# Kernel tuning notes

Measured on AMD Instinct MI355X. Metric: run time of the kernel, lower is better.

The kernel has to match this reference:

```python
import jax, jax.numpy as jnp
import numpy as np

B, S, D = 8, 2048, 768
H1 = 512
EMBED_DIM = 768  # scale = sqrt(embed_dim)


def setup_inputs() -> dict:
    key = jax.random.key(0)
    ks = jax.random.split(key, 5)
    q = jax.random.normal(ks[0], (B, S, D), dtype=jnp.float32)
    k = jax.random.normal(ks[1], (B, S, D), dtype=jnp.float32)
    v = jax.random.normal(ks[2], (B, S, D), dtype=jnp.float32)
    W1 = jax.random.normal(ks[3], (D, H1), dtype=jnp.float32) * (1.0 / np.sqrt(D))
    b1 = jnp.zeros((H1,), dtype=jnp.float32)
    W2 = jax.random.normal(ks[4], (H1, 1), dtype=jnp.float32) * (1.0 / np.sqrt(H1))
    b2 = jnp.zeros((1,), dtype=jnp.float32)
    return {"q": q, "k": k, "v": v, "W1": W1, "b1": b1, "W2": W2, "b2": b2}


def reference(q, k, v, W1, b1, W2, b2):
    # MLP gate on v: fc2(tanh(fc1(v))) -> [B, S, 1] -> squeeze -> [B, S]
    g = jnp.tanh(v @ W1 + b1) @ W2 + b2          # [B, S, 1]
    g = g[..., 0][:, None, :]                    # unsqueeze(-2): [B, 1, S]

    # scores scaled by sqrt(seq_len) (q.shape[1]), as in the original
    scores = jnp.einsum("bqd,bkd->bqk", q, k) / jnp.sqrt(
        jnp.asarray(q.shape[1], dtype=q.dtype))  # [B, S, S]

    # first softmax over dim=1 (column-wise over query axis)
    s = jax.nn.softmax(scores, axis=1)           # [B, S, S]

    # blend with column-mean, scale by sqrt(embed_dim)
    s_mean = jnp.mean(s, axis=1, keepdims=True)  # [B, 1, S]
    scale = jnp.sqrt(jnp.asarray(EMBED_DIM, dtype=q.dtype))
    attn_scores = (s * (1.0 - g) + s_mean * g) / scale

    # second softmax over last dim; dropout p=0 is identity
    attn_weights = jax.nn.softmax(attn_scores, axis=-1)

    attn_output = jnp.einsum("bqk,bkd->bqd", attn_weights, v) + q
    return attn_output, attn_weights
```

## Files before the change

### kernel.cpp

```cpp
#include <hip/hip_runtime.h>

#define BATCH 8
#define SEQ   2048
#define DIM   768
#define HID   512

typedef __attribute__((ext_vector_type(8))) short  short8;
typedef __attribute__((ext_vector_type(4))) float  f32x4;

#define BAR()   asm volatile("s_barrier" ::: "memory")
#define WAITL0() asm volatile("s_waitcnt lgkmcnt(0)" ::: "memory")
#define VMC(n)  asm volatile("s_waitcnt vmcnt(" #n ")" ::: "memory")

__device__ __forceinline__ unsigned short f2bf(float f) {
  union { float f; unsigned u; } x; x.f = f;
  return (unsigned short)((x.u + 0x7FFFu + ((x.u >> 16) & 1u)) >> 16);
}
__device__ __forceinline__ float bf2f(unsigned short u) {
  union { unsigned u; float f; } x; x.u = ((unsigned)u) << 16;
  return x.f;
}
__device__ __forceinline__ void gll16(const void* g, void* l) {
  __builtin_amdgcn_global_load_lds(
      (const __attribute__((address_space(1))) void*)g,
      (__attribute__((address_space(3))) void*)l, 16, 0, 0);
}
__device__ __forceinline__ int swz2(int o) { return o ^ (((o >> 8) & 7) << 4); }
__device__ __forceinline__ int swz3(int o) { return o ^ (((o >> 7) & 7) << 4); }

template<int VAR>
__global__ __launch_bounds__(512, 2)
void gemm8(const unsigned short* __restrict__ Ap, const unsigned short* __restrict__ Bp,
           const float* __restrict__ qres, float* __restrict__ Cf)
{
  constexpr int K     = (VAR == 1) ? DIM : SEQ;
  constexpr int NT    = K / 64;
  constexpr int NITER = NT / 2;
  constexpr int APB   = (VAR == 1) ? DIM * 2 : SEQ * 2;
  constexpr int BPB   = (VAR == 1) ? 8192    : SEQ * 2;
  constexpr int GX    = (VAR == 1) ? 8 : 3;
  constexpr int GY    = 8;
  constexpr int NWG   = GX * GY * BATCH;

  __shared__ __align__(16) unsigned char LDS[131072];

  int wg = ((blockIdx.x & 7) * (NWG >> 3)) + ((int)blockIdx.x >> 3);
  const int z  = wg / (GX * GY);
  const int r2 = wg % (GX * GY);
  const int by = r2 / GX;
  const int bx = r2 % GX;
  const int brow = by * 256, bcol = bx * 256;

  const int tid  = threadIdx.x;
  const int lane = tid & 63, wid = tid >> 6;
  const int wm   = wid >> 2, wn = wid & 3;
  const int lhi  = lane >> 4, llo = lane & 15;

  const char* Abase;
  const char* Bbase;
  if constexpr (VAR == 1) {
    Abase = (const char*)(Ap + (size_t)z * SEQ * DIM) + (size_t)brow * APB;
    Bbase = (const char*)(Bp + (size_t)z * SEQ * 4096 + 2048) + (size_t)bcol * BPB;
  } else {
    Abase = (const char*)(Ap + (size_t)z * SEQ * SEQ) + (size_t)brow * APB;
    Bbase = (const char*)(Bp + (size_t)z * (size_t)DIM * SEQ) + (size_t)bcol * BPB;
  }

  int sr[2], sk[2];
  #pragma unroll
  for (int c = 0; c < 2; ++c) {
    int o = wid * 2048 + c * 1024 + lane * 16;
    int a = swz3(o);
    sr[c] = a >> 7; sk[c] = a & 127;
  }
  auto stA = [&](int buf, int hh, int t) {
    #pragma unroll
    for (int c = 0; c < 2; ++c)
      gll16(Abase + (size_t)(hh * 128 + sr[c]) * APB + t * 128 + sk[c],
            LDS + buf * 32768 + hh * 16384 + wid * 2048 + c * 1024);
  };
  auto stB = [&](int buf, int hh, int t) {
    #pragma unroll
    for (int c = 0; c < 2; ++c)
      gll16(Bbase + (size_t)(hh * 128 + sr[c]) * BPB + t * 128 + sk[c],
            LDS + 65536 + buf * 32768 + hh * 16384 + wid * 2048 + c * 1024);
  };

  f32x4 acc[8][4];
  #pragma unroll
  for (int m = 0; m < 8; ++m)
    #pragma unroll
    for (int n = 0; n < 4; ++n)
      acc[m][n] = (f32x4)(0.0f);

  stA(0, 0, 0); stA(0, 1, 0); stB(0, 0, 0); stB(0, 1, 0);
  stB(1, 0, 1); stB(1, 1, 1);
  VMC(4);
  BAR();

  auto ITER = [&](int i, bool last) {
    #pragma unroll
    for (int kk = 0; kk < 2; ++kk) {
      const int buf = kk;
      short8 aR[4][2], b0R[2][2], b1R[2][2];
      #pragma unroll
      for (int ph = 0; ph < 4; ++ph) {
        const int h  = ph >> 1;
        const int nh = (ph == 1 || ph == 2) ? 1 : 0;
        if (ph == 0 || ph == 2) {
          #pragma unroll
          for (int fm = 0; fm < 4; ++fm)
            #pragma unroll
            for (int kh = 0; kh < 2; ++kh) {
              int o = (wm * 128 + h * 64 + fm * 16 + llo) * 128 + kh * 64 + lhi * 16;
              aR[fm][kh] = *(const short8*)(LDS + buf * 32768 + swz3(o));
            }
        }
        if (ph == 0) {
          #pragma unroll
          for (int fn = 0; fn < 2; ++fn)
            #pragma unroll
            for (int kh = 0; kh < 2; ++kh) {
              int o = (wn * 64 + fn * 16 + llo) * 128 + kh * 64 + lhi * 16;
              b0R[fn][kh] = *(const short8*)(LDS + 65536 + buf * 32768 + swz3(o));
            }
        }
        if (ph == 1) {
          #pragma unroll
          for (int fn = 0; fn < 2; ++fn)
            #pragma unroll
            for (int kh = 0; kh < 2; ++kh) {
              int o = (wn * 64 + 32 + fn * 16 + llo) * 128 + kh * 64 + lhi * 16;
              b1R[fn][kh] = *(const short8*)(LDS + 65536 + buf * 32768 + swz3(o));
            }
        }
        const int P = kk * 4 + ph;
        if      (P == 0) stA(1, 0, 2 * i + 1);
        else if (P == 1) stA(1, 1, 2 * i + 1);
        else if (P == 2) { if (!last) stB(0, 0, 2 * i + 2); }
        else if (P == 3) { if (!last) stB(0, 1, 2 * i + 2); }
        else if (P == 4) { if (!last) stA(0, 0, 2 * i + 2); }
        else if (P == 5) { if (!last) stA(0, 1, 2 * i + 2); }
        else if (P == 6) { if (!last) stB(1, 0, 2 * i + 3); }
        else if (P == 7) { if (!last) stB(1, 1, 2 * i + 3); }
        if (P == 3) { if (last) { VMC(0); } else { VMC(4); } }
        if (P == 7) { if (!last) { VMC(4); } }
        BAR();
        WAITL0();
        __builtin_amdgcn_sched_barrier(0);
        __builtin_amdgcn_s_setprio(1);
        #pragma unroll
        for (int kh = 0; kh < 2; ++kh)
          #pragma unroll
          for (int fm = 0; fm < 4; ++fm)
            #pragma unroll
            for (int fn = 0; fn < 2; ++fn)
              acc[h * 4 + fm][nh * 2 + fn] = __builtin_amdgcn_mfma_f32_16x16x32_bf16(
                  aR[fm][kh], nh ? b1R[fn][kh] : b0R[fn][kh],
                  acc[h * 4 + fm][nh * 2 + fn], 0, 0, 0);
        __builtin_amdgcn_s_setprio(0);
        BAR();
      }
    }
  };

  for (int i = 0; i < NITER - 1; ++i) ITER(i, false);
  ITER(NITER - 1, true);

  if constexpr (VAR == 1) {
    const float rs = 0.02209708691207961f;
    unsigned short* C16 = reinterpret_cast<unsigned short*>(Cf);
    #pragma unroll
    for (int FM = 0; FM < 8; ++FM)
      #pragma unroll
      for (int r = 0; r < 4; ++r) {
        size_t R = (size_t)z * SEQ + (brow + wm * 128 + FM * 16 + lhi * 4 + r);
        #pragma unroll
        for (int FN = 0; FN < 4; ++FN) {
          int col = bcol + wn * 64 + FN * 16 + llo;
          C16[R * 4096 + col] = f2bf(acc[FM][FN][r] * rs);
        }
      }
  }
  if constexpr (VAR == 2) {
    float* C = Cf + (size_t)z * SEQ * DIM;
    const float* Q = qres + (size_t)z * SEQ * DIM;
    #pragma unroll
    for (int FM = 0; FM < 8; ++FM)
      #pragma unroll
      for (int r = 0; r < 4; ++r) {
        int rowg = brow + wm * 128 + FM * 16 + lhi * 4 + r;
        #pragma unroll
        for (int FN = 0; FN < 4; ++FN) {
          int colg = bcol + wn * 64 + FN * 16 + llo;
          C[(size_t)rowg * DIM + colg] = acc[FM][FN][r] + Q[(size_t)rowg * DIM + colg];
        }
      }
  }
}

__global__ __launch_bounds__(256)
void gemm_gate(const unsigned short* __restrict__ Ab, const unsigned short* __restrict__ Bb,
               const float* __restrict__ bias, const float* __restrict__ W2,
               float* __restrict__ pg)
{
  constexpr int K = DIM, NT = K / 32, APITCH = 4096, BPITCH = DIM;
  constexpr int GX = 4, NWG = 512;

  __shared__ __align__(16) unsigned short AsL[2 * 128 * 32];
  __shared__ __align__(16) unsigned short BsL[2 * 128 * 32];
  __shared__ float gred[128][2];

  int wg = blockIdx.x;
  wg = (wg & 7) * (NWG >> 3) + (wg >> 3);
  const int bx = wg % GX;
  const int by = wg / GX;

  const int tid  = threadIdx.x;
  const int brow = by * 128;
  const int bcol = bx * 128;
  const int lane = tid & 63;
  const int wid  = tid >> 6;
  const int wr   = (wid >> 1) * 64;
  const int wc   = (wid & 1) * 64;
  const int lhi  = lane >> 4;
  const int llo  = lane & 15;

  const unsigned short* Asrc = Ab + (size_t)brow * APITCH;
  const unsigned short* Bsrc = Bb + (size_t)bcol * BPITCH;

  f32x4 acc[4][4];
  #pragma unroll
  for (int m = 0; m < 4; ++m)
    #pragma unroll
    for (int n = 0; n < 4; ++n)
      acc[m][n] = (f32x4)(0.0f);

  auto stage = [&](int buf, int k0) {
    #pragma unroll
    for (int i = 0; i < 2; ++i) {
      int ob = wid * 2048 + i * 1024;
      int a  = swz2(ob + lane * 16);
      gll16((const char*)Asrc + (size_t)(a >> 6) * (APITCH * 2) + (size_t)k0 * 2 + (a & 63),
            (char*)AsL + buf * 8192 + ob);
    }
    #pragma unroll
    for (int i = 0; i < 2; ++i) {
      int ob = wid * 2048 + i * 1024;
      int a  = swz2(ob + lane * 16);
      gll16((const char*)Bsrc + (size_t)(a >> 6) * (BPITCH * 2) + (size_t)k0 * 2 + (a & 63),
            (char*)BsL + buf * 8192 + ob);
    }
  };

  stage(0, 0);
  for (int t = 0; t < NT; ++t) {
    if (t + 1 < NT) {
      stage((t + 1) & 1, (t + 1) * 32);
      VMC(4);
    } else {
      VMC(0);
    }
    BAR();
    __builtin_amdgcn_sched_barrier(0);

    const int bb = (t & 1) * 8192;
    short8 af[4], bfr[4];
    #pragma unroll
    for (int m = 0; m < 4; ++m) {
      int a = (wr + m * 16 + llo) * 64 + lhi * 16;
      af[m] = *(const short8*)((const char*)AsL + bb + swz2(a));
    }
    #pragma unroll
    for (int n = 0; n < 4; ++n) {
      int a = (wc + n * 16 + llo) * 64 + lhi * 16;
      bfr[n] = *(const short8*)((const char*)BsL + bb + swz2(a));
    }
    #pragma unroll
    for (int m = 0; m < 4; ++m)
      #pragma unroll
      for (int n = 0; n < 4; ++n)
        acc[m][n] = __builtin_amdgcn_mfma_f32_16x16x32_bf16(af[m], bfr[n], acc[m][n], 0, 0, 0);

    __builtin_amdgcn_sched_barrier(0);
    BAR();
    __builtin_amdgcn_sched_barrier(0);
  }

  #pragma unroll
  for (int m = 0; m < 4; ++m) {
    #pragma unroll
    for (int r = 0; r < 4; ++r) {
      int lrow = wr + m * 16 + lhi * 4 + r;
      float part = 0.f;
      #pragma unroll
      for (int n = 0; n < 4; ++n) {
        int colg = bcol + wc + n * 16 + llo;
        float t = tanhf(acc[m][n][r] + bias[colg]);
        part += t * W2[colg];
      }
      part += __shfl_xor(part, 1);
      part += __shfl_xor(part, 2);
      part += __shfl_xor(part, 4);
      part += __shfl_xor(part, 8);
      if (llo == 0) gred[lrow][wid & 1] = part;
    }
  }
  __syncthreads();
  if (tid < 128)
    pg[(size_t)bx * 16384 + brow + tid] = gred[tid][0] + gred[tid][1];
}

__global__ __launch_bounds__(256)
void gemm_slow(const float* __restrict__ Wf, const float* __restrict__ Vf,
               const float* __restrict__ qres, float* __restrict__ Cf)
{
  __shared__ __align__(16) unsigned short AsL[128 * 64];
  __shared__ __align__(16) unsigned short BsL[128 * 32];

  const int tid  = threadIdx.x;
  const int z    = blockIdx.z;
  const int brow = blockIdx.y * 128;
  const int bcol = blockIdx.x * 128;
  const int lane = tid & 63;
  const int wid  = tid >> 6;
  const int wr   = (wid >> 1) * 64;
  const int wc   = (wid & 1) * 64;
  const int lhi  = lane >> 4;
  const int llo  = lane & 15;

  const float* AsrcF = Wf + (size_t)z * SEQ * SEQ + (size_t)brow * SEQ;
  const float* BsrcF = Vf + (size_t)z * SEQ * DIM;

  f32x4 acc[4][4];
  #pragma unroll
  for (int m = 0; m < 4; ++m)
    #pragma unroll
    for (int n = 0; n < 4; ++n)
      acc[m][n] = (f32x4)(0.0f);

  for (int k0 = 0; k0 < SEQ; k0 += 32) {
    #pragma unroll
    for (int i = 0; i < 4; ++i) {
      int ob = wid * 4096 + i * 1024;
      int a  = swz3(ob + lane * 16);
      gll16((const char*)AsrcF + (size_t)(a >> 7) * (SEQ * 4) + (size_t)k0 * 4 + (a & 127),
            (char*)AsL + ob);
    }
    {
      int n4 = (tid & 31) << 2;
      int kb = (tid >> 5) << 2;
      float4 r0 = *(const float4*)(BsrcF + (size_t)(k0 + kb + 0) * DIM + bcol + n4);
      float4 r1 = *(const float4*)(BsrcF + (size_t)(k0 + kb + 1) * DIM + bcol + n4);
      float4 r2 = *(const float4*)(BsrcF + (size_t)(k0 + kb + 2) * DIM + bcol + n4);
      float4 r3 = *(const float4*)(BsrcF + (size_t)(k0 + kb + 3) * DIM + bcol + n4);
      float a0[4] = {r0.x, r0.y, r0.z, r0.w};
      float a1[4] = {r1.x, r1.y, r1.z, r1.w};
      float a2[4] = {r2.x, r2.y, r2.z, r2.w};
      float a3[4] = {r3.x, r3.y, r3.z, r3.w};
      #pragma unroll
      for (int jj = 0; jj < 4; ++jj) {
        unsigned lo = (__float_as_uint(a0[jj]) >> 16) | (__float_as_uint(a1[jj]) & 0xFFFF0000u);
        unsigned hi = (__float_as_uint(a2[jj]) >> 16) | (__float_as_uint(a3[jj]) & 0xFFFF0000u);
        int ol = (n4 + jj) * 64 + kb * 2;
        *(uint2*)((char*)BsL + swz2(ol)) = make_uint2(lo, hi);
      }
    }
    __syncthreads();

    short8 af[4], bfr[4];
    #pragma unroll
    for (int m = 0; m < 4; ++m) {
      int row = wr + m * 16 + llo;
      int a0i = row * 128 + lhi * 32;
      f32x4 x = *(const f32x4*)((const char*)AsL + swz3(a0i));
      f32x4 y = *(const f32x4*)((const char*)AsL + swz3(a0i + 16));
      union { unsigned u[4]; short8 s; } r;
      r.u[0] = (__float_as_uint(x[0]) >> 16) | (__float_as_uint(x[1]) & 0xFFFF0000u);
      r.u[1] = (__float_as_uint(x[2]) >> 16) | (__float_as_uint(x[3]) & 0xFFFF0000u);
      r.u[2] = (__float_as_uint(y[0]) >> 16) | (__float_as_uint(y[1]) & 0xFFFF0000u);
      r.u[3] = (__float_as_uint(y[2]) >> 16) | (__float_as_uint(y[3]) & 0xFFFF0000u);
      af[m] = r.s;
    }
    #pragma unroll
    for (int n = 0; n < 4; ++n) {
      int a = (wc + n * 16 + llo) * 64 + lhi * 16;
      bfr[n] = *(const short8*)((const char*)BsL + swz2(a));
    }
    #pragma unroll
    for (int m = 0; m < 4; ++m)
      #pragma unroll
      for (int n = 0; n < 4; ++n)
        acc[m][n] = __builtin_amdgcn_mfma_f32_16x16x32_bf16(af[m], bfr[n], acc[m][n], 0, 0, 0);
    __syncthreads();
  }

  float* C = Cf + (size_t)z * SEQ * DIM;
  const float* Q = qres + (size_t)z * SEQ * DIM;
  #pragma unroll
  for (int m = 0; m < 4; ++m)
    #pragma unroll
    for (int r = 0; r < 4; ++r) {
      int rowg = brow + wr + m * 16 + lhi * 4 + r;
      #pragma unroll
      for (int n = 0; n < 4; ++n) {
        int colg = bcol + wc + n * 16 + llo;
        C[(size_t)rowg * DIM + colg] = acc[m][n][r] + Q[(size_t)rowg * DIM + colg];
      }
    }
}

__global__ __launch_bounds__(256)
void prepack(const float* __restrict__ q, const float* __restrict__ k,
             const float* __restrict__ v, unsigned short* __restrict__ qb,
             unsigned short* __restrict__ wsl)
{
  const int NT = (BATCH * SEQ * DIM) / 4;
  for (int i = blockIdx.x * 256 + threadIdx.x; i < NT; i += 2048 * 256) {
    int e = i * 4;
    float4 qv = *(const float4*)(q + e);
    float4 kv = *(const float4*)(k + e);
    float4 vv = *(const float4*)(v + e);
    ushort4 qo; qo.x = f2bf(qv.x); qo.y = f2bf(qv.y); qo.z = f2bf(qv.z); qo.w = f2bf(qv.w);
    ushort4 ko; ko.x = f2bf(kv.x); ko.y = f2bf(kv.y); ko.z = f2bf(kv.z); ko.w = f2bf(kv.w);
    ushort4 vo; vo.x = f2bf(vv.x); vo.y = f2bf(vv.y); vo.z = f2bf(vv.z); vo.w = f2bf(vv.w);
    *(ushort4*)(qb + e) = qo;
    int r = e / DIM, c = e % DIM;
    size_t off = (size_t)r * 4096 + 2048 + c;
    *(ushort4*)(wsl + off) = ko;
    *(ushort4*)(wsl + off + DIM) = vo;
  }
}

__global__ __launch_bounds__(256)
void transpose_f32_bf16(const float* __restrict__ src, unsigned short* __restrict__ dst,
                        int R, int C)
{
  __shared__ unsigned short T[64][65];
  const float* s = src + (size_t)blockIdx.z * R * C;
  unsigned short* d = dst + (size_t)blockIdx.z * R * C;
  int r0 = blockIdx.y * 64, c0 = blockIdx.x * 64;
  int tr = threadIdx.x >> 6, tc = threadIdx.x & 63;
  #pragma unroll
  for (int j = 0; j < 16; ++j) {
    int row = j * 4 + tr;
    T[row][tc] = f2bf(s[(size_t)(r0 + row) * C + c0 + tc]);
  }
  __syncthreads();
  #pragma unroll
  for (int j = 0; j < 16; ++j) {
    int row = j * 4 + tr;
    d[(size_t)(c0 + row) * R + r0 + tc] = T[tc][row];
  }
}

__global__ void g_combine(const float* __restrict__ pg, const float* __restrict__ b2,
                          float* __restrict__ g)
{
  int i = blockIdx.x * 256 + threadIdx.x;
  g[i] = b2[0] + pg[i] + pg[16384 + i] + pg[2 * 16384 + i] + pg[3 * 16384 + i];
}

__global__ __launch_bounds__(256)
void colstat_part(const unsigned short* __restrict__ sc, float* __restrict__ pl)
{
  const int gc = blockIdx.x * 256 + threadIdx.x;
  const int b = gc >> 11, c = gc & 2047;
  const unsigned short* p = sc + (size_t)b * SEQ * 4096 + c;
  const int q0 = blockIdx.y * 128;
  float l = 0.f;
  #pragma unroll 4
  for (int qq = q0; qq < q0 + 128; ++qq) l += __expf(bf2f(p[(size_t)qq * 4096]));
  pl[blockIdx.y * 16384 + gc] = l;
}

__global__ void colstat_comb(const float* __restrict__ pl, float* __restrict__ lcol)
{
  int gc = blockIdx.x * 256 + threadIdx.x;
  float l = 0.f;
  #pragma unroll
  for (int ch = 0; ch < 16; ++ch) l += pl[ch * 16384 + gc];
  lcol[gc] = l;
}

template<bool FAST>
__global__ __launch_bounds__(256)
void rowpass(float* __restrict__ w, const float* __restrict__ lcol,
             const float* __restrict__ gg, unsigned short* __restrict__ wb)
{
  const size_t row = blockIdx.x;
  const int b = (int)(row >> 11);
  const unsigned short* p = (const unsigned short*)w + row * 4096;
  float* wrow = w + row * 2048;
  const int c0 = threadIdx.x * 8;
  const float* lc = lcol + (b << 11);
  const float* gb = gg + (b << 11);

  unsigned short xs[8];
  *(ushort4*)&xs[0] = *(const ushort4*)(p + c0);
  *(ushort4*)&xs[4] = *(const ushort4*)(p + c0 + 4);
  float ls[8], gs[8];
  *(float4*)&ls[0] = *(const float4*)(lc + c0);
  *(float4*)&ls[4] = *(const float4*)(lc + c0 + 4);
  *(float4*)&gs[0] = *(const float4*)(gb + c0);
  *(float4*)&gs[4] = *(const float4*)(gb + c0 + 4);

  float e[8];
  float psum = 0.f;
  #pragma unroll
  for (int j = 0; j < 8; ++j) {
    float s = __expf(bf2f(xs[j])) / ls[j];
    float t = (s * (1.f - gs[j]) + gs[j] * (1.f / 2048.f)) * 0.03608439182435161f;
    float ev = __expf(t);
    e[j] = ev;
    psum += ev;
  }
  #pragma unroll
  for (int off = 1; off < 64; off <<= 1) psum += __shfl_xor(psum, off);
  __shared__ float red[4];
  if ((threadIdx.x & 63) == 0) red[threadIdx.x >> 6] = psum;
  __syncthreads();
  float inv = 1.f / (red[0] + red[1] + red[2] + red[3]);
  float4 o0, o1;
  o0.x = e[0] * inv; o0.y = e[1] * inv; o0.z = e[2] * inv; o0.w = e[3] * inv;
  o1.x = e[4] * inv; o1.y = e[5] * inv; o1.z = e[6] * inv; o1.w = e[7] * inv;
  *(float4*)(wrow + c0) = o0;
  *(float4*)(wrow + c0 + 4) = o1;
  if constexpr (FAST) {
    ushort4 b0, b1v;
    b0.x = f2bf(o0.x); b0.y = f2bf(o0.y); b0.z = f2bf(o0.z); b0.w = f2bf(o0.w);
    b1v.x = f2bf(o1.x); b1v.y = f2bf(o1.y); b1v.z = f2bf(o1.z); b1v.w = f2bf(o1.w);
    *(ushort4*)(wb + row * 2048 + c0) = b0;
    *(ushort4*)(wb + row * 2048 + c0 + 4) = b1v;
  }
}

extern "C" void kernel_launch(void* const* d_in, const int* in_sizes, int n_in,
                              void* d_out, int out_size, void* d_ws, size_t ws_size,
                              hipStream_t stream)
{
  (void)in_sizes; (void)n_in; (void)out_size;
  const float* q  = (const float*)d_in[0];
  const float* k  = (const float*)d_in[1];
  const float* v  = (const float*)d_in[2];
  const float* W1 = (const float*)d_in[3];
  const float* b1 = (const float*)d_in[4];
  const float* W2 = (const float*)d_in[5];
  const float* b2 = (const float*)d_in[6];

  float* out0 = (float*)d_out;
  float* wbuf = out0 + (size_t)BATCH * SEQ * DIM;
  unsigned short* wsl = (unsigned short*)wbuf;
  unsigned short* qb  = (unsigned short*)out0;

  float* g    = (float*)d_ws;
  float* lcol = g + 16384;
  float* pg   = lcol + 16384;
  float* pl   = pg + 65536;
  unsigned short* W1T = (unsigned short*)(pl + 262144);
  unsigned short* vT  = (unsigned short*)((char*)d_ws + 2228224);
  unsigned short* wb  = vT + (size_t)12582912;
  const bool fast = ws_size >= 94502912ull;

  prepack<<<2048, 256, 0, stream>>>(q, k, v, qb, wsl);
  transpose_f32_bf16<<<dim3(8, 12, 1), 256, 0, stream>>>(W1, W1T, 768, 512);
  if (fast)
    transpose_f32_bf16<<<dim3(12, 32, 8), 256, 0, stream>>>(v, vT, 2048, 768);

  gemm_gate<<<512, 256, 0, stream>>>(wsl + 2816, W1T, b1, W2, pg);
  g_combine<<<64, 256, 0, stream>>>(pg, b2, g);

  gemm8<1><<<512, 512, 0, stream>>>(qb, wsl, nullptr, wbuf);

  colstat_part<<<dim3(64, 16), 256, 0, stream>>>(wsl, pl);
  colstat_comb<<<64, 256, 0, stream>>>(pl, lcol);

  if (fast) {
    rowpass<true><<<16384, 256, 0, stream>>>(wbuf, lcol, g, wb);
    gemm8<2><<<192, 512, 0, stream>>>(wb, vT, q, out0);
  } else {
    rowpass<false><<<16384, 256, 0, stream>>>(wbuf, lcol, g, nullptr);
    gemm_slow<<<dim3(6, 16, 8), 256, 0, stream>>>(wbuf, v, q, out0);
  }
}
```

Baseline: 274.9 us.

## Fuse column exp-sums into score GEMM epilogue and v transpose into prepack

Computes the per-column exp-sum partials inside the score GEMM epilogue from the rounded bf16 values, removing the separate strided column-statistics kernels. The v transpose to bf16 is folded into the prepack kernel so v is read only once. The MLP gate GEMM is reimplemented via the 256x256-tile gemm8 template with a tanh/W2 reduction epilogue, and the bias/partial combine kernels are merged into one finalize kernel. Costs include extra epilogue work and LDS syncs in the main GEMM, and fewer workgroups (128) for the gate GEMM.

```diff
diff --git a/kernel.cpp b/kernel.cpp
--- a/kernel.cpp
+++ b/kernel.cpp
@@ -8,9 +8,9 @@
 typedef __attribute__((ext_vector_type(8))) short  short8;
 typedef __attribute__((ext_vector_type(4))) float  f32x4;
 
-#define BAR()   asm volatile("s_barrier" ::: "memory")
+#define BAR()    asm volatile("s_barrier" ::: "memory")
 #define WAITL0() asm volatile("s_waitcnt lgkmcnt(0)" ::: "memory")
-#define VMC(n)  asm volatile("s_waitcnt vmcnt(" #n ")" ::: "memory")
+#define VMC(n)   asm volatile("s_waitcnt vmcnt(" #n ")" ::: "memory")
 
 __device__ __forceinline__ unsigned short f2bf(float f) {
   union { float f; unsigned u; } x; x.f = f;
@@ -31,16 +31,19 @@
 template<int VAR>
 __global__ __launch_bounds__(512, 2)
 void gemm8(const unsigned short* __restrict__ Ap, const unsigned short* __restrict__ Bp,
-           const float* __restrict__ qres, float* __restrict__ Cf)
-{
-  constexpr int K     = (VAR == 1) ? DIM : SEQ;
+           const float* __restrict__ qres, float* __restrict__ Cf,
+           const float* __restrict__ bias, const float* __restrict__ W2,
+           float* __restrict__ pg, float* __restrict__ pl)
+{
+  constexpr int K     = (VAR == 2) ? SEQ : DIM;
   constexpr int NT    = K / 64;
   constexpr int NITER = NT / 2;
-  constexpr int APB   = (VAR == 1) ? DIM * 2 : SEQ * 2;
-  constexpr int BPB   = (VAR == 1) ? 8192    : SEQ * 2;
-  constexpr int GX    = (VAR == 1) ? 8 : 3;
-  constexpr int GY    = 8;
-  constexpr int NWG   = GX * GY * BATCH;
+  constexpr int APB   = (VAR == 0) ? 8192 : (VAR == 1 ? 1536 : 4096);
+  constexpr int BPB   = (VAR == 0) ? 1536 : (VAR == 1 ? 8192 : 4096);
+  constexpr int GX    = (VAR == 0) ? 2 : (VAR == 1 ? 8 : 3);
+  constexpr int GY    = (VAR == 0) ? 64 : 8;
+  constexpr int NB    = (VAR == 0) ? 1 : BATCH;
+  constexpr int NWG   = GX * GY * NB;
 
   __shared__ __align__(16) unsigned char LDS[131072];
 
@@ -58,7 +61,10 @@
 
   const char* Abase;
   const char* Bbase;
-  if constexpr (VAR == 1) {
+  if constexpr (VAR == 0) {
+    Abase = (const char*)Ap + (size_t)brow * APB;
+    Bbase = (const char*)Bp + (size_t)bcol * BPB;
+  } else if constexpr (VAR == 1) {
     Abase = (const char*)(Ap + (size_t)z * SEQ * DIM) + (size_t)brow * APB;
     Bbase = (const char*)(Bp + (size_t)z * SEQ * 4096 + 2048) + (size_t)bcol * BPB;
   } else {
@@ -167,9 +173,37 @@
   for (int i = 0; i < NITER - 1; ++i) ITER(i, false);
   ITER(NITER - 1, true);
 
+  if constexpr (VAR == 0) {
+    float* gredF = (float*)LDS;
+    float b1v[4], w2v[4];
+    #pragma unroll
+    for (int FN = 0; FN < 4; ++FN) {
+      int colg = bcol + wn * 64 + FN * 16 + llo;
+      b1v[FN] = bias[colg]; w2v[FN] = W2[colg];
+    }
+    #pragma unroll
+    for (int FM = 0; FM < 8; ++FM)
+      #pragma unroll
+      for (int r = 0; r < 4; ++r) {
+        float part = 0.f;
+        #pragma unroll
+        for (int FN = 0; FN < 4; ++FN)
+          part += tanhf(acc[FM][FN][r] + b1v[FN]) * w2v[FN];
+        part += __shfl_xor(part, 1);
+        part += __shfl_xor(part, 2);
+        part += __shfl_xor(part, 4);
+        part += __shfl_xor(part, 8);
+        if (llo == 0) gredF[(wm * 128 + FM * 16 + lhi * 4 + r) * 4 + wn] = part;
+      }
+    __syncthreads();
+    if (tid < 256)
+      pg[(size_t)bx * 16384 + brow + tid] =
+          gredF[tid * 4 + 0] + gredF[tid * 4 + 1] + gredF[tid * 4 + 2] + gredF[tid * 4 + 3];
+  }
   if constexpr (VAR == 1) {
     const float rs = 0.02209708691207961f;
     unsigned short* C16 = reinterpret_cast<unsigned short*>(Cf);
+    float cs[4] = {0.f, 0.f, 0.f, 0.f};
     #pragma unroll
     for (int FM = 0; FM < 8; ++FM)
       #pragma unroll
@@ -178,9 +212,21 @@
         #pragma unroll
         for (int FN = 0; FN < 4; ++FN) {
           int col = bcol + wn * 64 + FN * 16 + llo;
-          C16[R * 4096 + col] = f2bf(acc[FM][FN][r] * rs);
+          unsigned short us = f2bf(acc[FM][FN][r] * rs);
+          C16[R * 4096 + col] = us;
+          cs[FN] += __expf(bf2f(us));
         }
       }
+    float* cp = (float*)LDS;
+    #pragma unroll
+    for (int FN = 0; FN < 4; ++FN) {
+      cs[FN] += __shfl_xor(cs[FN], 16);
+      cs[FN] += __shfl_xor(cs[FN], 32);
+      if (lhi == 0) cp[wm * 256 + wn * 64 + FN * 16 + llo] = cs[FN];
+    }
+    __syncthreads();
+    if (tid < 256)
+      pl[(size_t)by * 16384 + z * 2048 + bcol + tid] = cp[tid] + cp[256 + tid];
   }
   if constexpr (VAR == 2) {
     float* C = Cf + (size_t)z * SEQ * DIM;
@@ -197,118 +243,6 @@
         }
       }
   }
-}
-
-__global__ __launch_bounds__(256)
-void gemm_gate(const unsigned short* __restrict__ Ab, const unsigned short* __restrict__ Bb,
-               const float* __restrict__ bias, const float* __restrict__ W2,
-               float* __restrict__ pg)
-{
-  constexpr int K = DIM, NT = K / 32, APITCH = 4096, BPITCH = DIM;
-  constexpr int GX = 4, NWG = 512;
-
-  __shared__ __align__(16) unsigned short AsL[2 * 128 * 32];
-  __shared__ __align__(16) unsigned short BsL[2 * 128 * 32];
-  __shared__ float gred[128][2];
-
-  int wg = blockIdx.x;
-  wg = (wg & 7) * (NWG >> 3) + (wg >> 3);
-  const int bx = wg % GX;
-  const int by = wg / GX;
-
-  const int tid  = threadIdx.x;
-  const int brow = by * 128;
-  const int bcol = bx * 128;
-  const int lane = tid & 63;
-  const int wid  = tid >> 6;
-  const int wr   = (wid >> 1) * 64;
-  const int wc   = (wid & 1) * 64;
-  const int lhi  = lane >> 4;
-  const int llo  = lane & 15;
-
-  const unsigned short* Asrc = Ab + (size_t)brow * APITCH;
-  const unsigned short* Bsrc = Bb + (size_t)bcol * BPITCH;
-
-  f32x4 acc[4][4];
-  #pragma unroll
-  for (int m = 0; m < 4; ++m)
-    #pragma unroll
-    for (int n = 0; n < 4; ++n)
-      acc[m][n] = (f32x4)(0.0f);
-
-  auto stage = [&](int buf, int k0) {
-    #pragma unroll
-    for (int i = 0; i < 2; ++i) {
-      int ob = wid * 2048 + i * 1024;
-      int a  = swz2(ob + lane * 16);
-      gll16((const char*)Asrc + (size_t)(a >> 6) * (APITCH * 2) + (size_t)k0 * 2 + (a & 63),
-            (char*)AsL + buf * 8192 + ob);
-    }
-    #pragma unroll
-    for (int i = 0; i < 2; ++i) {
-      int ob = wid * 2048 + i * 1024;
-      int a  = swz2(ob + lane * 16);
-      gll16((const char*)Bsrc + (size_t)(a >> 6) * (BPITCH * 2) + (size_t)k0 * 2 + (a & 63),
-            (char*)BsL + buf * 8192 + ob);
-    }
-  };
-
-  stage(0, 0);
-  for (int t = 0; t < NT; ++t) {
-    if (t + 1 < NT) {
-      stage((t + 1) & 1, (t + 1) * 32);
-      VMC(4);
-    } else {
-      VMC(0);
-    }
-    BAR();
-    __builtin_amdgcn_sched_barrier(0);
-
-    const int bb = (t & 1) * 8192;
-    short8 af[4], bfr[4];
-    #pragma unroll
-    for (int m = 0; m < 4; ++m) {
-      int a = (wr + m * 16 + llo) * 64 + lhi * 16;
-      af[m] = *(const short8*)((const char*)AsL + bb + swz2(a));
-    }
-    #pragma unroll
-    for (int n = 0; n < 4; ++n) {
-      int a = (wc + n * 16 + llo) * 64 + lhi * 16;
-      bfr[n] = *(const short8*)((const char*)BsL + bb + swz2(a));
-    }
-    #pragma unroll
-    for (int m = 0; m < 4; ++m)
-      #pragma unroll
-      for (int n = 0; n < 4; ++n)
-        acc[m][n] = __builtin_amdgcn_mfma_f32_16x16x32_bf16(af[m], bfr[n], acc[m][n], 0, 0, 0);
-
-    __builtin_amdgcn_sched_barrier(0);
-    BAR();
-    __builtin_amdgcn_sched_barrier(0);
-  }
-
-  #pragma unroll
-  for (int m = 0; m < 4; ++m) {
-    #pragma unroll
-    for (int r = 0; r < 4; ++r) {
-      int lrow = wr + m * 16 + lhi * 4 + r;
-      float part = 0.f;
-      #pragma unroll
-      for (int n = 0; n < 4; ++n) {
-        int colg = bcol + wc + n * 16 + llo;
-        float t = tanhf(acc[m][n][r] + bias[colg]);
-        part += t * W2[colg];
-      }
-      part += __shfl_xor(part, 1);
-      part += __shfl_xor(part, 2);
-      part += __shfl_xor(part, 4);
-      part += __shfl_xor(part, 8);
-      if (llo == 0) gred[lrow][wid & 1] = part;
-    }
-  }
-  __syncthreads();
-  if (tid < 128)
-    pg[(size_t)bx * 16384 + brow + tid] = gred[tid][0] + gred[tid][1];
 }
 
 __global__ __launch_bounds__(256)
@@ -411,13 +345,21 @@
 }
 
 __global__ __launch_bounds__(256)
-void prepack(const float* __restrict__ q, const float* __restrict__ k,
-             const float* __restrict__ v, unsigned short* __restrict__ qb,
-             unsigned short* __restrict__ wsl)
-{
-  const int NT = (BATCH * SEQ * DIM) / 4;
-  for (int i = blockIdx.x * 256 + threadIdx.x; i < NT; i += 2048 * 256) {
-    int e = i * 4;
+void prepack_fused(const float* __restrict__ q, const float* __restrict__ k,
+                   const float* __restrict__ v, unsigned short* __restrict__ qb,
+                   unsigned short* __restrict__ wsl, unsigned short* __restrict__ vT,
+                   int dovT)
+{
+  __shared__ unsigned short T[64][66];
+  const int z  = blockIdx.z;
+  const int r0 = blockIdx.y * 64, c0 = blockIdx.x * 64;
+  const size_t mb = (size_t)z * SEQ * DIM;
+  const int t16 = threadIdx.x & 15, trw = threadIdx.x >> 4;
+
+  #pragma unroll
+  for (int j = 0; j < 4; ++j) {
+    int row = j * 16 + trw;
+    size_t e = mb + (size_t)(r0 + row) * DIM + c0 + t16 * 4;
     float4 qv = *(const float4*)(q + e);
     float4 kv = *(const float4*)(k + e);
     float4 vv = *(const float4*)(v + e);
@@ -425,10 +367,21 @@
     ushort4 ko; ko.x = f2bf(kv.x); ko.y = f2bf(kv.y); ko.z = f2bf(kv.z); ko.w = f2bf(kv.w);
     ushort4 vo; vo.x = f2bf(vv.x); vo.y = f2bf(vv.y); vo.z = f2bf(vv.z); vo.w = f2bf(vv.w);
     *(ushort4*)(qb + e) = qo;
-    int r = e / DIM, c = e % DIM;
-    size_t off = (size_t)r * 4096 + 2048 + c;
-    *(ushort4*)(wsl + off) = ko;
-    *(ushort4*)(wsl + off + DIM) = vo;
+    size_t so = (size_t)(z * SEQ + r0 + row) * 4096 + 2048 + c0 + t16 * 4;
+    *(ushort4*)(wsl + so) = ko;
+    *(ushort4*)(wsl + so + DIM) = vo;
+    *(unsigned*)&T[row][t16 * 4]     = (unsigned)vo.x | ((unsigned)vo.y << 16);
+    *(unsigned*)&T[row][t16 * 4 + 2] = (unsigned)vo.z | ((unsigned)vo.w << 16);
+  }
+  __syncthreads();
+  if (dovT) {
+    const int tc = threadIdx.x & 63, tr2 = threadIdx.x >> 6;
+    unsigned short* vTm = vT + (size_t)z * DIM * SEQ;
+    #pragma unroll
+    for (int j = 0; j < 16; ++j) {
+      int orow = j * 4 + tr2;
+      vTm[(size_t)(c0 + orow) * SEQ + r0 + tc] = T[tc][orow];
+    }
   }
 }
 
@@ -437,50 +390,31 @@
                         int R, int C)
 {
   __shared__ unsigned short T[64][65];
-  const float* s = src + (size_t)blockIdx.z * R * C;
-  unsigned short* d = dst + (size_t)blockIdx.z * R * C;
   int r0 = blockIdx.y * 64, c0 = blockIdx.x * 64;
   int tr = threadIdx.x >> 6, tc = threadIdx.x & 63;
   #pragma unroll
   for (int j = 0; j < 16; ++j) {
     int row = j * 4 + tr;
-    T[row][tc] = f2bf(s[(size_t)(r0 + row) * C + c0 + tc]);
+    T[row][tc] = f2bf(src[(size_t)(r0 + row) * C + c0 + tc]);
   }
   __syncthreads();
   #pragma unroll
   for (int j = 0; j < 16; ++j) {
     int row = j * 4 + tr;
-    d[(size_t)(c0 + row) * R + r0 + tc] = T[tc][row];
-  }
-}
-
-__global__ void g_combine(const float* __restrict__ pg, const float* __restrict__ b2,
-                          float* __restrict__ g)
+    dst[(size_t)(c0 + row) * R + r0 + tc] = T[tc][row];
+  }
+}
+
+__global__ void finalize(const float* __restrict__ pl, const float* __restrict__ pg,
+                         const float* __restrict__ b2, float* __restrict__ lcol,
+                         float* __restrict__ g)
 {
   int i = blockIdx.x * 256 + threadIdx.x;
-  g[i] = b2[0] + pg[i] + pg[16384 + i] + pg[2 * 16384 + i] + pg[3 * 16384 + i];
-}
-
-__global__ __launch_bounds__(256)
-void colstat_part(const unsigned short* __restrict__ sc, float* __restrict__ pl)
-{
-  const int gc = blockIdx.x * 256 + threadIdx.x;
-  const int b = gc >> 11, c = gc & 2047;
-  const unsigned short* p = sc + (size_t)b * SEQ * 4096 + c;
-  const int q0 = blockIdx.y * 128;
   float l = 0.f;
-  #pragma unroll 4
-  for (int qq = q0; qq < q0 + 128; ++qq) l += __expf(bf2f(p[(size_t)qq * 4096]));
-  pl[blockIdx.y * 16384 + gc] = l;
-}
-
-__global__ void colstat_comb(const float* __restrict__ pl, float* __restrict__ lcol)
-{
-  int gc = blockIdx.x * 256 + threadIdx.x;
-  float l = 0.f;
-  #pragma unroll
-  for (int ch = 0; ch < 16; ++ch) l += pl[ch * 16384 + gc];
-  lcol[gc] = l;
+  #pragma unroll
+  for (int ch = 0; ch < 8; ++ch) l += pl[ch * 16384 + i];
+  lcol[i] = l;
+  g[i] = b2[0] + pg[i] + pg[16384 + i];
 }
 
 template<bool FAST>
@@ -562,22 +496,17 @@
   unsigned short* wb  = vT + (size_t)12582912;
   const bool fast = ws_size >= 94502912ull;
 
-  prepack<<<2048, 256, 0, stream>>>(q, k, v, qb, wsl);
+  prepack_fused<<<dim3(12, 32, 8), 256, 0, stream>>>(q, k, v, qb, wsl, vT, fast ? 1 : 0);
   transpose_f32_bf16<<<dim3(8, 12, 1), 256, 0, stream>>>(W1, W1T, 768, 512);
-  if (fast)
-    transpose_f32_bf16<<<dim3(12, 32, 8), 256, 0, stream>>>(v, vT, 2048, 768);
-
-  gemm_gate<<<512, 256, 0, stream>>>(wsl + 2816, W1T, b1, W2, pg);
-  g_combine<<<64, 256, 0, stream>>>(pg, b2, g);
-
-  gemm8<1><<<512, 512, 0, stream>>>(qb, wsl, nullptr, wbuf);
-
-  colstat_part<<<dim3(64, 16), 256, 0, stream>>>(wsl, pl);
-  colstat_comb<<<64, 256, 0, stream>>>(pl, lcol);
+
+  gemm8<0><<<128, 512, 0, stream>>>(wsl + 2816, W1T, nullptr, nullptr, b1, W2, pg, nullptr);
+  gemm8<1><<<512, 512, 0, stream>>>(qb, wsl, nullptr, wbuf, nullptr, nullptr, nullptr, pl);
+
+  finalize<<<64, 256, 0, stream>>>(pl, pg, b2, lcol, g);
 
   if (fast) {
     rowpass<true><<<16384, 256, 0, stream>>>(wbuf, lcol, g, wb);
-    gemm8<2><<<192, 512, 0, stream>>>(wb, vT, q, out0);
+    gemm8<2><<<192, 512, 0, stream>>>(wb, vT, q, out0, nullptr, nullptr, nullptr, nullptr);
   } else {
     rowpass<false><<<16384, 256, 0, stream>>>(wbuf, lcol, g, nullptr);
     gemm_slow<<<dim3(6, 16, 8), 256, 0, stream>>>(wbuf, v, q, out0);
```

Result: faster. 260.9 us (-5.1%).
